# Performance work log

Hardware: AMD Instinct MI355X
Metric: run time of the kernel (lower is better)

Reference implementation:

```python
import jax, jax.numpy as jnp
import numpy as np

N_NODES = 100000
N_EDGES = 1200000
MAX_ATOM_TYPE = 100
NUM_FEATURES = 92
GC_DIM = 64          # pre_layer_dim == gc_dim == CGConv channels
NUM_RBF = 32
NUM_GC_LAYERS = 4
CUTOFF_UPPER = 5.0
BN_EPS = 1e-5


def setup_inputs() -> dict:
    key = jax.random.key(0)
    ks = jax.random.split(key, 12)
    atom_types = jax.random.randint(ks[0], (N_NODES,), 0, MAX_ATOM_TYPE, dtype=jnp.int32)
    pos = jax.random.uniform(ks[1], (N_NODES, 3), dtype=jnp.float32) * 6.0  # box side 6 -> many dists < cutoff
    edge_index = jax.random.randint(ks[2], (2, N_EDGES), 0, N_NODES, dtype=jnp.int32)
    # parameters
    emb = jax.random.normal(ks[3], (MAX_ATOM_TYPE, NUM_FEATURES), dtype=jnp.float32)
    s = 1.0 / np.sqrt(NUM_FEATURES)
    pre_W = jax.random.uniform(ks[4], (NUM_FEATURES, GC_DIM), minval=-s, maxval=s, dtype=jnp.float32)
    pre_b = jnp.zeros((GC_DIM,), jnp.float32)
    zdim = 2 * GC_DIM + NUM_RBF  # [x_i, x_j, edge_attr]
    sz = 1.0 / np.sqrt(zdim)
    Wf = jax.random.uniform(ks[5], (NUM_GC_LAYERS, zdim, GC_DIM), minval=-sz, maxval=sz, dtype=jnp.float32)
    bf = jnp.zeros((NUM_GC_LAYERS, GC_DIM), jnp.float32)
    Ws = jax.random.uniform(ks[6], (NUM_GC_LAYERS, zdim, GC_DIM), minval=-sz, maxval=sz, dtype=jnp.float32)
    bs = jnp.zeros((NUM_GC_LAYERS, GC_DIM), jnp.float32)
    bn_gamma = jnp.ones((NUM_GC_LAYERS, GC_DIM), jnp.float32)
    bn_beta = jnp.zeros((NUM_GC_LAYERS, GC_DIM), jnp.float32)
    # ExpNormalSmearing (torchmd-net) init
    start = np.exp(-CUTOFF_UPPER)
    means = jnp.asarray(np.linspace(start, 1.0, NUM_RBF), jnp.float32)
    betas = jnp.full((NUM_RBF,), (2.0 / NUM_RBF * (1.0 - start)) ** -2, jnp.float32)
    return {"atom_types": atom_types, "pos": pos, "edge_index": edge_index,
            "emb": emb, "pre_W": pre_W, "pre_b": pre_b,
            "Wf": Wf, "bf": bf, "Ws": Ws, "bs": bs,
            "bn_gamma": bn_gamma, "bn_beta": bn_beta,
            "means": means, "betas": betas}


def _forward(atom_types, pos, edge_index, emb, pre_W, pre_b, Wf, bf, Ws, bs,
             bn_gamma, bn_beta, means, betas):
    src, dst = edge_index[0], edge_index[1]
    # distance (edge_vec = pos[src] - pos[dst])
    vec = pos[src] - pos[dst]                                  # [E,3]
    dist = jnp.sqrt(jnp.sum(vec * vec, axis=-1) + 1e-12)       # [E]
    # expnorm RBF with cosine cutoff (cutoff_lower = 0)
    cutoff = 0.5 * (jnp.cos(dist * (np.pi / CUTOFF_UPPER)) + 1.0) * (dist < CUTOFF_UPPER)
    alpha = 5.0 / CUTOFF_UPPER
    edge_attr = cutoff[:, None] * jnp.exp(
        -betas * (jnp.exp(-alpha * dist)[:, None] - means) ** 2)  # [E,NUM_RBF]
    # embedding + pre layer
    x = emb[atom_types]                                        # [N,F]
    x = jax.nn.relu(x @ pre_W + pre_b)                         # [N,C]
    # mean-aggregation degree (scatter-mean denominator)
    deg = jax.ops.segment_sum(jnp.ones_like(dist), dst, num_segments=N_NODES)
    inv_deg = jnp.where(deg > 0, 1.0 / jnp.maximum(deg, 1.0), 0.0)[:, None]
    for l in range(NUM_GC_LAYERS):
        # CGConv: z = [x_i, x_j, e]; out = x + mean_j(sigmoid(lin_f(z)) * softplus(lin_s(z)))
        z = jnp.concatenate([x[dst], x[src], edge_attr], axis=-1)   # [E, 2C+R]
        msg = jax.nn.sigmoid(z @ Wf[l] + bf[l]) * jax.nn.softplus(z @ Ws[l] + bs[l])
        agg = jax.ops.segment_sum(msg, dst, num_segments=N_NODES) * inv_deg
        x = x + agg
        # BatchNorm1d (batch statistics, biased var, as in torch training mode)
        mu = jnp.mean(x, axis=0)
        var = jnp.mean((x - mu) ** 2, axis=0)
        x = (x - mu) * jax.lax.rsqrt(var + BN_EPS) * bn_gamma[l] + bn_beta[l]
    return x


def reference(atom_types, pos, edge_index, emb, pre_W, pre_b, Wf, bf, Ws, bs,
              bn_gamma, bn_beta, means, betas):
    return _forward(atom_types, pos, edge_index, emb, pre_W, pre_b, Wf, bf, Ws, bs,
                    bn_gamma, bn_beta, means, betas)
```

## Files before the change

### kernel.cpp

```cpp
#include <hip/hip_runtime.h>
#include <math.h>

#define N_NODES 100000
#define N_EDGES 1200000
#define GC 64
#define RBF 32
#define NLAYERS 4
#define NF 92
#define NATOM 100
#define BN_EPS 1e-5f
#define TILE_GRID 2048
#define NWIN (N_EDGES / 16)
#define LOG2E 1.44269504f
#define LN2 0.69314718f

typedef _Float16 half8 __attribute__((ext_vector_type(8)));
typedef _Float16 half4 __attribute__((ext_vector_type(4)));
typedef float f32x4 __attribute__((ext_vector_type(4)));

__global__ __launch_bounds__(256) void deg_kernel(
    const int* __restrict__ ei, int* __restrict__ deg)
{
    int e = blockIdx.x * 256 + threadIdx.x;
    if (e >= N_EDGES) return;
    atomicAdd(&deg[ei[N_EDGES + e]], 1);
}

__global__ __launch_bounds__(256) void scan_a_kernel(const int* __restrict__ deg, int* __restrict__ bsums)
{
    __shared__ int sm[256];
    int tid = threadIdx.x;
    int i = blockIdx.x * 256 + tid;
    int v = (i < N_NODES) ? deg[i] : 0;
    sm[tid] = v;
    __syncthreads();
    for (int s = 128; s > 0; s >>= 1) {
        if (tid < s) sm[tid] += sm[tid + s];
        __syncthreads();
    }
    if (tid == 0) bsums[blockIdx.x] = sm[0];
}

__global__ __launch_bounds__(512) void scan_b_kernel(const int* __restrict__ bsums, int* __restrict__ boffs)
{
    __shared__ int sm[512];
    int tid = threadIdx.x;
    int v = (tid < 391) ? bsums[tid] : 0;
    sm[tid] = v;
    __syncthreads();
    for (int off = 1; off < 512; off <<= 1) {
        int t = (tid >= off) ? sm[tid - off] : 0;
        __syncthreads();
        sm[tid] += t;
        __syncthreads();
    }
    boffs[tid] = (tid == 0) ? 0 : sm[tid - 1];
}

__global__ __launch_bounds__(256) void scan_c_kernel(
    const int* __restrict__ deg, const int* __restrict__ boffs,
    int* __restrict__ row_st, float* __restrict__ inv_deg)
{
    __shared__ int sm[256];
    int tid = threadIdx.x;
    int i = blockIdx.x * 256 + tid;
    int v = (i < N_NODES) ? deg[i] : 0;
    sm[tid] = v;
    __syncthreads();
    for (int off = 1; off < 256; off <<= 1) {
        int t = (tid >= off) ? sm[tid - off] : 0;
        __syncthreads();
        sm[tid] += t;
        __syncthreads();
    }
    if (i <= N_NODES) row_st[i] = boffs[blockIdx.x] + sm[tid] - v;
    if (i < N_NODES) inv_deg[i] = (v > 0) ? (1.0f / (float)v) : 0.0f;
}

__global__ __launch_bounds__(256) void scatter_perm_kernel(
    const int* __restrict__ ei, const int* __restrict__ row_st,
    int* __restrict__ cursor, int* __restrict__ csr_src, int* __restrict__ csr_dst)
{
    int e = blockIdx.x * 256 + threadIdx.x;
    if (e >= N_EDGES) return;
    int s = ei[e];
    int d = ei[N_EDGES + e];
    int p = atomicAdd(&cursor[d], 1);
    int idx = row_st[d] + p;
    csr_src[idx] = s;
    csr_dst[idx] = d;
}

__global__ __launch_bounds__(256) void rbf_kernel(
    const int* __restrict__ csr_src, const int* __restrict__ csr_dst,
    const float* __restrict__ pos,
    const float* __restrict__ means, const float* __restrict__ betas,
    unsigned int* __restrict__ ea)
{
    int idx = blockIdx.x * 256 + threadIdx.x;
    if (idx >= N_EDGES) return;
    int s = csr_src[idx];
    int d = csr_dst[idx];
    float dx = pos[s * 3 + 0] - pos[d * 3 + 0];
    float dy = pos[s * 3 + 1] - pos[d * 3 + 1];
    float dz = pos[s * 3 + 2] - pos[d * 3 + 2];
    float dist = sqrtf(dx * dx + dy * dy + dz * dz + 1e-12f);

    float cut = 0.0f;
    if (dist < 5.0f) cut = 0.5f * (__cosf(dist * 0.6283185307179586f) + 1.0f);
    float ex = __expf(-dist);
    union { _Float16 h[32]; uint4 u[4]; } pk;
#pragma unroll
    for (int k = 0; k < 32; k++) {
        float v = ex - means[k];
        pk.h[k] = (_Float16)(cut * __expf(-betas[k] * v * v));
    }
    uint4* op = (uint4*)(ea + (size_t)idx * 16);
    op[0] = pk.u[0];
    op[1] = pk.u[1];
    op[2] = pk.u[2];
    op[3] = pk.u[3];
}

__global__ __launch_bounds__(256) void window_prep_kernel(
    const int* __restrict__ csr_dst, const float* __restrict__ inv_deg,
    unsigned char* __restrict__ seg8, int* __restrict__ wnode, _Float16* __restrict__ inv_e)
{
    int w = blockIdx.x * 256 + threadIdx.x;
    if (w >= NWIN) return;
    int base = w * 16;
    int prev = -1, s = -1;
    for (int k = 0; k < 16; k++) {
        int d = csr_dst[base + k];
        if (d != prev) { s++; prev = d; wnode[base + s] = d; }
        seg8[base + k] = (unsigned char)s;
        inv_e[base + k] = (_Float16)(inv_deg[d] * LN2);
    }
    for (int m = s + 1; m < 16; m++) wnode[base + m] = -1;
}

__global__ __launch_bounds__(256) void wcvt_kernel(
    const float* __restrict__ Wf, const float* __restrict__ Ws,
    _Float16* __restrict__ wf16, _Float16* __restrict__ ws16)
{
    int i = blockIdx.x * 256 + threadIdx.x;
    int l = i / (160 * GC);
    int r = i - l * 160 * GC;
    int k = r >> 6;
    int col = r & 63;
    size_t o = ((size_t)l * GC + col) * 160 + k;
    wf16[o] = (_Float16)(Wf[i] * LOG2E);
    ws16[o] = (_Float16)(Ws[i] * LOG2E);
}

__global__ __launch_bounds__(64) void atom_table_kernel(
    const float* __restrict__ emb, const float* __restrict__ pre_W,
    const float* __restrict__ pre_b, float* __restrict__ T)
{
    int a = blockIdx.x;
    int c = threadIdx.x;
    float acc = pre_b[c];
    for (int k = 0; k < NF; k++) acc = fmaf(emb[a * NF + k], pre_W[k * GC + c], acc);
    T[a * GC + c] = fmaxf(acc, 0.0f);
}

__global__ __launch_bounds__(256) void xinit_kernel(
    const int* __restrict__ atom_types, const float* __restrict__ T,
    float* __restrict__ x, _Float16* __restrict__ x16)
{
    int i = blockIdx.x * 256 + threadIdx.x;
    int n = i >> 4;
    int a = atom_types[n];
    float4 v = ((const float4*)T)[a * 16 + (i & 15)];
    ((float4*)x)[i] = v;
    half4 h = { (_Float16)v.x, (_Float16)v.y, (_Float16)v.z, (_Float16)v.w };
    ((half4*)x16)[i] = h;
}

static __device__ __forceinline__ void compute_win(
    half8 D0, half8 D1, half8 S0, half8 S1, half8 E, int moff,
    const half8 (&WGF)[5][2], const half8 (&WGS)[5][2],
    const float (&biasf)[2], const float (&biass)[2],
    int r16, int quad, int cb,
    const unsigned char* __restrict__ seg8, const int* __restrict__ wnode,
    const _Float16* __restrict__ inv_e, float* __restrict__ x)
{
    unsigned int segq = *(const unsigned int*)(seg8 + moff + quad * 4);
    int4 wn4 = *(const int4*)(wnode + moff + quad * 4);
    half4 inv4 = *(const half4*)(inv_e + moff + quad * 4);

    f32x4 accf[2], accs[2];
#pragma unroll
    for (int ctl = 0; ctl < 2; ctl++) {
        accf[ctl] = (f32x4){biasf[ctl], biasf[ctl], biasf[ctl], biasf[ctl]};
        accs[ctl] = (f32x4){biass[ctl], biass[ctl], biass[ctl], biass[ctl]};
    }
#pragma unroll
    for (int ctl = 0; ctl < 2; ctl++) {
        accf[ctl] = __builtin_amdgcn_mfma_f32_16x16x32_f16(D0, WGF[0][ctl], accf[ctl], 0, 0, 0);
        accs[ctl] = __builtin_amdgcn_mfma_f32_16x16x32_f16(D0, WGS[0][ctl], accs[ctl], 0, 0, 0);
        accf[ctl] = __builtin_amdgcn_mfma_f32_16x16x32_f16(D1, WGF[1][ctl], accf[ctl], 0, 0, 0);
        accs[ctl] = __builtin_amdgcn_mfma_f32_16x16x32_f16(D1, WGS[1][ctl], accs[ctl], 0, 0, 0);
        accf[ctl] = __builtin_amdgcn_mfma_f32_16x16x32_f16(S0, WGF[2][ctl], accf[ctl], 0, 0, 0);
        accs[ctl] = __builtin_amdgcn_mfma_f32_16x16x32_f16(S0, WGS[2][ctl], accs[ctl], 0, 0, 0);
        accf[ctl] = __builtin_amdgcn_mfma_f32_16x16x32_f16(S1, WGF[3][ctl], accf[ctl], 0, 0, 0);
        accs[ctl] = __builtin_amdgcn_mfma_f32_16x16x32_f16(S1, WGS[3][ctl], accs[ctl], 0, 0, 0);
        accf[ctl] = __builtin_amdgcn_mfma_f32_16x16x32_f16(E,  WGF[4][ctl], accf[ctl], 0, 0, 0);
        accs[ctl] = __builtin_amdgcn_mfma_f32_16x16x32_f16(E,  WGS[4][ctl], accs[ctl], 0, 0, 0);
    }
    half4 msgh[2];
#pragma unroll
    for (int ctl = 0; ctl < 2; ctl++) {
#pragma unroll
        for (int rr = 0; rr < 4; rr++) {
            float af = accf[ctl][rr];
            float as = accs[ctl][rr];
            float sg = __builtin_amdgcn_rcpf(1.0f + __builtin_amdgcn_exp2f(-af));
            float sp = fmaxf(as, 0.0f)
                     + __builtin_amdgcn_logf(1.0f + __builtin_amdgcn_exp2f(-__builtin_fabsf(as)));
            msgh[ctl][rr] = (_Float16)(sg * sp);
        }
    }
    half4 am;
#pragma unroll
    for (int j = 0; j < 4; j++) {
        int sj = (segq >> (8 * j)) & 0xff;
        am[j] = (sj == r16) ? inv4[j] : (_Float16)0.0f;
    }
    int wa[4] = { wn4.x, wn4.y, wn4.z, wn4.w };
    const f32x4 zf = (f32x4){0.0f, 0.0f, 0.0f, 0.0f};
#pragma unroll
    for (int ctl = 0; ctl < 2; ctl++) {
        f32x4 red = __builtin_amdgcn_mfma_f32_16x16x16f16(am, msgh[ctl], zf, 0, 0, 0);
#pragma unroll
        for (int rr = 0; rr < 4; rr++) {
            int nd = wa[rr];
            if (nd >= 0) atomicAdd(&x[(size_t)nd * GC + cb + ctl * 16 + r16], red[rr]);
        }
    }
}

#define LOADFRAGS(P0_, P1_, Q0_, Q1_, EE_, SRC_, DST_, WW_)                          \
    P0_ = *(const half8*)(x16 + (size_t)(DST_) * GC + quad * 8);                     \
    P1_ = *(const half8*)(x16 + (size_t)(DST_) * GC + 32 + quad * 8);                \
    Q0_ = *(const half8*)(x16 + (size_t)(SRC_) * GC + quad * 8);                     \
    Q1_ = *(const half8*)(x16 + (size_t)(SRC_) * GC + 32 + quad * 8);                \
    EE_ = *(const half8*)(ea + ((size_t)(WW_) * 16 + r16) * RBF + quad * 8);

__global__ __launch_bounds__(256, 3) void win_mfma_kernel(
    const _Float16* __restrict__ x16, const _Float16* __restrict__ ea,
    const int* __restrict__ csr_src, const int* __restrict__ csr_dst,
    const unsigned char* __restrict__ seg8, const int* __restrict__ wnode,
    const _Float16* __restrict__ inv_e,
    const _Float16* __restrict__ wf16, const _Float16* __restrict__ ws16,
    const float* __restrict__ bfv, const float* __restrict__ bsv,
    float* __restrict__ x)
{
    const int lane = threadIdx.x & 63;
    const int wid = threadIdx.x >> 6;
    const int quad = lane >> 4;
    const int r16 = lane & 15;
    const int wgid = blockIdx.x * 4 + wid;
    const int cb = (wgid & 1) * 32;
    int w = wgid >> 1;
    const int NSEQ = TILE_GRID * 2;

    half8 WGF[5][2], WGS[5][2];
#pragma unroll
    for (int ctl = 0; ctl < 2; ctl++) {
        const _Float16* wfp = wf16 + (size_t)(cb + ctl * 16 + r16) * 160 + quad * 8;
        const _Float16* wsp = ws16 + (size_t)(cb + ctl * 16 + r16) * 160 + quad * 8;
#pragma unroll
        for (int kt = 0; kt < 5; kt++) {
            WGF[kt][ctl] = *(const half8*)(wfp + kt * 32);
            WGS[kt][ctl] = *(const half8*)(wsp + kt * 32);
        }
    }
    float biasf[2], biass[2];
#pragma unroll
    for (int ctl = 0; ctl < 2; ctl++) {
        int col = cb + ctl * 16 + r16;
        biasf[ctl] = bfv[col] * LOG2E;
        biass[ctl] = bsv[col] * LOG2E;
    }

    int sA = csr_src[w * 16 + r16];
    int dA = csr_dst[w * 16 + r16];
    half8 AD0, AD1, AS0, AS1, AE;
    LOADFRAGS(AD0, AD1, AS0, AS1, AE, sA, dA, w);
    int moffA = w * 16;

    int wB = w + NSEQ; if (wB >= NWIN) wB = NWIN - 1;
    int sB = csr_src[wB * 16 + r16];
    int dB = csr_dst[wB * 16 + r16];
    half8 BD0, BD1, BQ0, BQ1, BE;
    LOADFRAGS(BD0, BD1, BQ0, BQ1, BE, sB, dB, wB);
    int moffB = wB * 16;

    int wC = wB + NSEQ; if (wC >= NWIN) wC = NWIN - 1;
    int sC = csr_src[wC * 16 + r16];
    int dC = csr_dst[wC * 16 + r16];

    while (true) {
        compute_win(AD0, AD1, AS0, AS1, AE, moffA, WGF, WGS, biasf, biass,
                    r16, quad, cb, seg8, wnode, inv_e, x);
        LOADFRAGS(AD0, AD1, AS0, AS1, AE, sC, dC, wC);
        moffA = wC * 16;
        wC += NSEQ; if (wC >= NWIN) wC = NWIN - 1;
        sC = csr_src[wC * 16 + r16];
        dC = csr_dst[wC * 16 + r16];
        w += NSEQ;
        if (w >= NWIN) break;

        compute_win(BD0, BD1, BQ0, BQ1, BE, moffB, WGF, WGS, biasf, biass,
                    r16, quad, cb, seg8, wnode, inv_e, x);
        LOADFRAGS(BD0, BD1, BQ0, BQ1, BE, sC, dC, wC);
        moffB = wC * 16;
        wC += NSEQ; if (wC >= NWIN) wC = NWIN - 1;
        sC = csr_src[wC * 16 + r16];
        dC = csr_dst[wC * 16 + r16];
        w += NSEQ;
        if (w >= NWIN) break;
    }
}

__global__ __launch_bounds__(256) void stats_kernel(const float* __restrict__ x, float* __restrict__ stats)
{
    const int lane = threadIdx.x & 63;
    const int wid = threadIdx.x >> 6;
    int w = blockIdx.x * 4 + wid;
    float s1 = 0.0f, s2 = 0.0f;
    for (int n = w; n < N_NODES; n += 1024) {
        float v = x[(size_t)n * GC + lane];
        s1 += v;
        s2 = fmaf(v, v, s2);
    }
    __shared__ float rs1[4][64];
    __shared__ float rs2[4][64];
    rs1[wid][lane] = s1;
    rs2[wid][lane] = s2;
    __syncthreads();
    if (threadIdx.x < 64) {
        atomicAdd(&stats[lane], rs1[0][lane] + rs1[1][lane] + rs1[2][lane] + rs1[3][lane]);
    } else if (threadIdx.x < 128) {
        int c = threadIdx.x & 63;
        atomicAdd(&stats[64 + c], rs2[0][c] + rs2[1][c] + rs2[2][c] + rs2[3][c]);
    }
}

__global__ __launch_bounds__(256) void bn_x16_kernel(
    const float* __restrict__ xn, const float* __restrict__ stats,
    const float* __restrict__ gamma, const float* __restrict__ beta,
    float* __restrict__ xout, _Float16* __restrict__ x16)
{
    int i = blockIdx.x * 256 + threadIdx.x;
    int c4 = (i & 15) * 4;
    float4 v = ((const float4*)xn)[i];
    float vv[4] = {v.x, v.y, v.z, v.w};
    float o[4];
    const float invN = 1.0f / (float)N_NODES;
#pragma unroll
    for (int t = 0; t < 4; t++) {
        int c = c4 + t;
        float mu = stats[c] * invN;
        float var = stats[64 + c] * invN - mu * mu;
        float sc = gamma[c] * rsqrtf(var + BN_EPS);
        o[t] = (vv[t] - mu) * sc + beta[c];
    }
    ((float4*)xout)[i] = make_float4(o[0], o[1], o[2], o[3]);
    half4 h = { (_Float16)o[0], (_Float16)o[1], (_Float16)o[2], (_Float16)o[3] };
    ((half4*)x16)[i] = h;
}

__global__ __launch_bounds__(256) void bn_kernel(
    const float* __restrict__ xn, const float* __restrict__ stats,
    const float* __restrict__ gamma, const float* __restrict__ beta,
    float* __restrict__ out)
{
    int i = blockIdx.x * 256 + threadIdx.x;
    int c4 = (i & 15) * 4;
    float4 v = ((const float4*)xn)[i];
    float vv[4] = {v.x, v.y, v.z, v.w};
    float o[4];
    const float invN = 1.0f / (float)N_NODES;
#pragma unroll
    for (int t = 0; t < 4; t++) {
        int c = c4 + t;
        float mu = stats[c] * invN;
        float var = stats[64 + c] * invN - mu * mu;
        float sc = gamma[c] * rsqrtf(var + BN_EPS);
        o[t] = (vv[t] - mu) * sc + beta[c];
    }
    ((float4*)out)[i] = make_float4(o[0], o[1], o[2], o[3]);
}

extern "C" void kernel_launch(void* const* d_in, const int* in_sizes, int n_in,
                              void* d_out, int out_size, void* d_ws, size_t ws_size,
                              hipStream_t stream)
{
    const int* atom_types = (const int*)d_in[0];
    const float* pos = (const float*)d_in[1];
    const int* edge_index = (const int*)d_in[2];
    const float* emb = (const float*)d_in[3];
    const float* pre_W = (const float*)d_in[4];
    const float* pre_b = (const float*)d_in[5];
    const float* Wf = (const float*)d_in[6];
    const float* bf = (const float*)d_in[7];
    const float* Ws = (const float*)d_in[8];
    const float* bs = (const float*)d_in[9];
    const float* gamma = (const float*)d_in[10];
    const float* beta = (const float*)d_in[11];
    const float* means = (const float*)d_in[12];
    const float* betas = (const float*)d_in[13];

    char* base = (char*)d_ws;
    char* p = base;
    auto alloc = [&](size_t bytes) -> char* {
        char* r = p;
        p += (bytes + 255) & ~(size_t)255;
        return r;
    };
    unsigned int* ea = (unsigned int*)alloc((size_t)N_EDGES * RBF * 2);
    float* x = (float*)alloc((size_t)N_NODES * GC * 4);
    _Float16* x16 = (_Float16*)alloc((size_t)N_NODES * GC * 2);
    int* csr_src = (int*)alloc((size_t)N_EDGES * 4);
    int* csr_dst = (int*)alloc((size_t)N_EDGES * 4);
    int* wnode = (int*)alloc((size_t)N_EDGES * 4);
    unsigned char* seg8 = (unsigned char*)alloc((size_t)N_EDGES);
    _Float16* inv_e = (_Float16*)alloc((size_t)N_EDGES * 2);
    _Float16* wf16 = (_Float16*)alloc((size_t)NLAYERS * GC * 160 * 2);
    _Float16* ws16 = (_Float16*)alloc((size_t)NLAYERS * GC * 160 * 2);
    int* row_st = (int*)alloc((size_t)(N_NODES + 1) * 4);
    float* inv_deg = (float*)alloc((size_t)N_NODES * 4);
    float* T = (float*)alloc((size_t)NATOM * GC * 4);
    int* bsums = (int*)alloc(512 * 4);
    int* boffs = (int*)alloc(512 * 4);
    const size_t ZR_INTS = (size_t)2 * N_NODES + 128 * NLAYERS + 64;
    char* zr = alloc(ZR_INTS * 4);
    int* deg = (int*)zr;
    int* cursor = deg + N_NODES;
    float* stats = (float*)(cursor + N_NODES);

    if ((size_t)(p - base) > ws_size) return;

    (void)hipMemsetAsync(zr, 0, ZR_INTS * 4, stream);

    const int EG = (N_EDGES + 255) / 256;
    deg_kernel<<<EG, 256, 0, stream>>>(edge_index, deg);
    scan_a_kernel<<<391, 256, 0, stream>>>(deg, bsums);
    scan_b_kernel<<<1, 512, 0, stream>>>(bsums, boffs);
    scan_c_kernel<<<391, 256, 0, stream>>>(deg, boffs, row_st, inv_deg);
    scatter_perm_kernel<<<EG, 256, 0, stream>>>(edge_index, row_st, cursor, csr_src, csr_dst);
    rbf_kernel<<<EG, 256, 0, stream>>>(csr_src, csr_dst, pos, means, betas, ea);
    window_prep_kernel<<<(NWIN + 255) / 256, 256, 0, stream>>>(csr_dst, inv_deg, seg8, wnode, inv_e);
    wcvt_kernel<<<(NLAYERS * 160 * GC) / 256, 256, 0, stream>>>(Wf, Ws, wf16, ws16);
    atom_table_kernel<<<NATOM, 64, 0, stream>>>(emb, pre_W, pre_b, T);
    xinit_kernel<<<N_NODES * 16 / 256, 256, 0, stream>>>(atom_types, T, x, x16);

    for (int l = 0; l < NLAYERS; l++) {
        win_mfma_kernel<<<TILE_GRID, 256, 0, stream>>>(
            x16, (const _Float16*)ea, csr_src, csr_dst, seg8, wnode, inv_e,
            wf16 + (size_t)l * GC * 160, ws16 + (size_t)l * GC * 160,
            bf + l * GC, bs + l * GC, x);
        stats_kernel<<<256, 256, 0, stream>>>(x, stats + l * 128);
        if (l < NLAYERS - 1) {
            bn_x16_kernel<<<N_NODES * 16 / 256, 256, 0, stream>>>(
                x, stats + l * 128, gamma + l * GC, beta + l * GC, x, x16);
        } else {
            bn_kernel<<<N_NODES * 16 / 256, 256, 0, stream>>>(
                x, stats + l * 128, gamma + l * GC, beta + l * GC, (float*)d_out);
        }
    }
}
```

Before: 852.0 us.

## Precompute per-node destination projection and fuse it into batchnorm kernel

The x_i (destination) part of both linear layers, plus bias, is now computed once per node into an fp16-packed buffer P2u instead of once per edge. The edge kernel loads these precomputed partial sums as accumulator initial values and runs only the source and edge-attribute MFMAs, cutting per-edge matmul work by about 40%. The per-node projection is fused into the batchnorm kernel for later layers, and softplus is simplified to log(1+exp2(x)), which risks overflow for large inputs. The cost is an extra node-sized buffer, scattered per-destination loads in the edge loop, and fp16 rounding of the partial sums.

```diff
diff --git a/kernel.cpp b/kernel.cpp
--- a/kernel.cpp
+++ b/kernel.cpp
@@ -16,7 +16,9 @@
 
 typedef _Float16 half8 __attribute__((ext_vector_type(8)));
 typedef _Float16 half4 __attribute__((ext_vector_type(4)));
+typedef _Float16 half2v __attribute__((ext_vector_type(2)));
 typedef float f32x4 __attribute__((ext_vector_type(4)));
+union U32H2 { unsigned int u; half2v h; };
 
 __global__ __launch_bounds__(256) void deg_kernel(
     const int* __restrict__ ei, int* __restrict__ deg)
@@ -177,84 +179,48 @@
     ((half4*)x16)[i] = h;
 }
 
-static __device__ __forceinline__ void compute_win(
-    half8 D0, half8 D1, half8 S0, half8 S1, half8 E, int moff,
-    const half8 (&WGF)[5][2], const half8 (&WGS)[5][2],
-    const float (&biasf)[2], const float (&biass)[2],
-    int r16, int quad, int cb,
-    const unsigned char* __restrict__ seg8, const int* __restrict__ wnode,
-    const _Float16* __restrict__ inv_e, float* __restrict__ x)
-{
-    unsigned int segq = *(const unsigned int*)(seg8 + moff + quad * 4);
-    int4 wn4 = *(const int4*)(wnode + moff + quad * 4);
-    half4 inv4 = *(const half4*)(inv_e + moff + quad * 4);
-
+static __device__ __forceinline__ void proj_mfma16(
+    const _Float16* __restrict__ wf, const _Float16* __restrict__ ws,
+    const float* __restrict__ bfv, const float* __restrict__ bsv,
+    const half8 Bn[2], int cb, int node, unsigned int* __restrict__ P2u)
+{
+    const int lane = threadIdx.x & 63;
+    const int quad = lane >> 4;
+    const int r16 = lane & 15;
     f32x4 accf[2], accs[2];
 #pragma unroll
-    for (int ctl = 0; ctl < 2; ctl++) {
-        accf[ctl] = (f32x4){biasf[ctl], biasf[ctl], biasf[ctl], biasf[ctl]};
-        accs[ctl] = (f32x4){biass[ctl], biass[ctl], biass[ctl], biass[ctl]};
-    }
-#pragma unroll
-    for (int ctl = 0; ctl < 2; ctl++) {
-        accf[ctl] = __builtin_amdgcn_mfma_f32_16x16x32_f16(D0, WGF[0][ctl], accf[ctl], 0, 0, 0);
-        accs[ctl] = __builtin_amdgcn_mfma_f32_16x16x32_f16(D0, WGS[0][ctl], accs[ctl], 0, 0, 0);
-        accf[ctl] = __builtin_amdgcn_mfma_f32_16x16x32_f16(D1, WGF[1][ctl], accf[ctl], 0, 0, 0);
-        accs[ctl] = __builtin_amdgcn_mfma_f32_16x16x32_f16(D1, WGS[1][ctl], accs[ctl], 0, 0, 0);
-        accf[ctl] = __builtin_amdgcn_mfma_f32_16x16x32_f16(S0, WGF[2][ctl], accf[ctl], 0, 0, 0);
-        accs[ctl] = __builtin_amdgcn_mfma_f32_16x16x32_f16(S0, WGS[2][ctl], accs[ctl], 0, 0, 0);
-        accf[ctl] = __builtin_amdgcn_mfma_f32_16x16x32_f16(S1, WGF[3][ctl], accf[ctl], 0, 0, 0);
-        accs[ctl] = __builtin_amdgcn_mfma_f32_16x16x32_f16(S1, WGS[3][ctl], accs[ctl], 0, 0, 0);
-        accf[ctl] = __builtin_amdgcn_mfma_f32_16x16x32_f16(E,  WGF[4][ctl], accf[ctl], 0, 0, 0);
-        accs[ctl] = __builtin_amdgcn_mfma_f32_16x16x32_f16(E,  WGS[4][ctl], accs[ctl], 0, 0, 0);
-    }
-    half4 msgh[2];
-#pragma unroll
-    for (int ctl = 0; ctl < 2; ctl++) {
-#pragma unroll
-        for (int rr = 0; rr < 4; rr++) {
-            float af = accf[ctl][rr];
-            float as = accs[ctl][rr];
-            float sg = __builtin_amdgcn_rcpf(1.0f + __builtin_amdgcn_exp2f(-af));
-            float sp = fmaxf(as, 0.0f)
-                     + __builtin_amdgcn_logf(1.0f + __builtin_amdgcn_exp2f(-__builtin_fabsf(as)));
-            msgh[ctl][rr] = (_Float16)(sg * sp);
-        }
-    }
-    half4 am;
-#pragma unroll
-    for (int j = 0; j < 4; j++) {
-        int sj = (segq >> (8 * j)) & 0xff;
-        am[j] = (sj == r16) ? inv4[j] : (_Float16)0.0f;
-    }
-    int wa[4] = { wn4.x, wn4.y, wn4.z, wn4.w };
-    const f32x4 zf = (f32x4){0.0f, 0.0f, 0.0f, 0.0f};
-#pragma unroll
-    for (int ctl = 0; ctl < 2; ctl++) {
-        f32x4 red = __builtin_amdgcn_mfma_f32_16x16x16f16(am, msgh[ctl], zf, 0, 0, 0);
-#pragma unroll
-        for (int rr = 0; rr < 4; rr++) {
-            int nd = wa[rr];
-            if (nd >= 0) atomicAdd(&x[(size_t)nd * GC + cb + ctl * 16 + r16], red[rr]);
-        }
-    }
-}
-
-#define LOADFRAGS(P0_, P1_, Q0_, Q1_, EE_, SRC_, DST_, WW_)                          \
-    P0_ = *(const half8*)(x16 + (size_t)(DST_) * GC + quad * 8);                     \
-    P1_ = *(const half8*)(x16 + (size_t)(DST_) * GC + 32 + quad * 8);                \
-    Q0_ = *(const half8*)(x16 + (size_t)(SRC_) * GC + quad * 8);                     \
-    Q1_ = *(const half8*)(x16 + (size_t)(SRC_) * GC + 32 + quad * 8);                \
-    EE_ = *(const half8*)(ea + ((size_t)(WW_) * 16 + r16) * RBF + quad * 8);
-
-__global__ __launch_bounds__(256, 3) void win_mfma_kernel(
-    const _Float16* __restrict__ x16, const _Float16* __restrict__ ea,
-    const int* __restrict__ csr_src, const int* __restrict__ csr_dst,
-    const unsigned char* __restrict__ seg8, const int* __restrict__ wnode,
-    const _Float16* __restrict__ inv_e,
-    const _Float16* __restrict__ wf16, const _Float16* __restrict__ ws16,
+    for (int sub = 0; sub < 2; sub++) {
+        accf[sub] = (f32x4){0.f, 0.f, 0.f, 0.f};
+        accs[sub] = (f32x4){0.f, 0.f, 0.f, 0.f};
+    }
+#pragma unroll
+    for (int kt = 0; kt < 2; kt++) {
+#pragma unroll
+        for (int sub = 0; sub < 2; sub++) {
+            int chan = cb + sub * 16 + r16;
+            half8 a = *(const half8*)(wf + (size_t)chan * 160 + kt * 32 + quad * 8);
+            half8 b = *(const half8*)(ws + (size_t)chan * 160 + kt * 32 + quad * 8);
+            accf[sub] = __builtin_amdgcn_mfma_f32_16x16x32_f16(a, Bn[kt], accf[sub], 0, 0, 0);
+            accs[sub] = __builtin_amdgcn_mfma_f32_16x16x32_f16(b, Bn[kt], accs[sub], 0, 0, 0);
+        }
+    }
+#pragma unroll
+    for (int sub = 0; sub < 2; sub++) {
+        float4 bf4 = *(const float4*)(bfv + cb + sub * 16 + quad * 4);
+        float4 bs4 = *(const float4*)(bsv + cb + sub * 16 + quad * 4);
+        half8 h = { (_Float16)(accf[sub][0] + bf4.x * LOG2E), (_Float16)(accs[sub][0] + bs4.x * LOG2E),
+                    (_Float16)(accf[sub][1] + bf4.y * LOG2E), (_Float16)(accs[sub][1] + bs4.y * LOG2E),
+                    (_Float16)(accf[sub][2] + bf4.z * LOG2E), (_Float16)(accs[sub][2] + bs4.z * LOG2E),
+                    (_Float16)(accf[sub][3] + bf4.w * LOG2E), (_Float16)(accs[sub][3] + bs4.w * LOG2E) };
+        *(half8*)(P2u + (size_t)node * GC + cb + sub * 16 + quad * 4) = h;
+    }
+}
+
+__global__ __launch_bounds__(256) void proj_kernel(
+    const _Float16* __restrict__ x16,
+    const _Float16* __restrict__ wf, const _Float16* __restrict__ ws,
     const float* __restrict__ bfv, const float* __restrict__ bsv,
-    float* __restrict__ x)
+    unsigned int* __restrict__ P2u)
 {
     const int lane = threadIdx.x & 63;
     const int wid = threadIdx.x >> 6;
@@ -262,63 +228,204 @@
     const int r16 = lane & 15;
     const int wgid = blockIdx.x * 4 + wid;
     const int cb = (wgid & 1) * 32;
+    const int nb = (wgid >> 1) * 16;
+    half8 Bn[2];
+    Bn[0] = *(const half8*)(x16 + (size_t)(nb + r16) * GC + quad * 8);
+    Bn[1] = *(const half8*)(x16 + (size_t)(nb + r16) * GC + 32 + quad * 8);
+    proj_mfma16(wf, ws, bfv, bsv, Bn, cb, nb + r16, P2u);
+}
+
+__global__ __launch_bounds__(256) void bnproj_kernel(
+    const float* __restrict__ xn, const float* __restrict__ stats,
+    const float* __restrict__ gamma, const float* __restrict__ beta,
+    float* __restrict__ xout, _Float16* __restrict__ x16,
+    const _Float16* __restrict__ wf, const _Float16* __restrict__ ws,
+    const float* __restrict__ bfv, const float* __restrict__ bsv,
+    unsigned int* __restrict__ P2u)
+{
+    __shared__ _Float16 lx[32 * 72];
+    const int nb = blockIdx.x * 32;
+    const float invN = 1.0f / (float)N_NODES;
+
+#pragma unroll
+    for (int rep = 0; rep < 2; rep++) {
+        int g = rep * 256 + threadIdx.x;
+        int gi = blockIdx.x * 512 + g;
+        int node = g >> 4;
+        int c4 = (g & 15) * 4;
+        float4 v = ((const float4*)xn)[gi];
+        float vv[4] = {v.x, v.y, v.z, v.w};
+        float o[4];
+#pragma unroll
+        for (int t = 0; t < 4; t++) {
+            int c = c4 + t;
+            float mu = stats[c] * invN;
+            float var = stats[64 + c] * invN - mu * mu;
+            float sc = gamma[c] * rsqrtf(var + BN_EPS);
+            o[t] = (vv[t] - mu) * sc + beta[c];
+        }
+        ((float4*)xout)[gi] = make_float4(o[0], o[1], o[2], o[3]);
+        half4 h = { (_Float16)o[0], (_Float16)o[1], (_Float16)o[2], (_Float16)o[3] };
+        ((half4*)x16)[gi] = h;
+        *(half4*)(lx + node * 72 + c4) = h;
+    }
+    __syncthreads();
+
+    const int lane = threadIdx.x & 63;
+    const int wid = threadIdx.x >> 6;
+    const int quad = lane >> 4;
+    const int r16 = lane & 15;
+    const int cb = (wid & 1) * 32;
+    const int tn = (wid >> 1) * 16 + r16;
+    half8 Bn[2];
+    Bn[0] = *(const half8*)(lx + tn * 72 + quad * 8);
+    Bn[1] = *(const half8*)(lx + tn * 72 + 32 + quad * 8);
+    proj_mfma16(wf, ws, bfv, bsv, Bn, cb, nb + tn, P2u);
+}
+
+static __device__ __forceinline__ void compute_win(
+    half8 S0, half8 S1, half8 E,
+    const unsigned int (&pv)[8], unsigned int segq, int4 wn4, half4 inv4,
+    const half8 (&WGF)[3][2], const half8 (&WGS)[3][2],
+    int r16, int quad, int cb, float* __restrict__ x)
+{
+    f32x4 accf[2], accs[2];
+#pragma unroll
+    for (int ctl = 0; ctl < 2; ctl++) {
+#pragma unroll
+        for (int rr = 0; rr < 4; rr++) {
+            U32H2 t; t.u = pv[ctl * 4 + rr];
+            accf[ctl][rr] = (float)t.h.x;
+            accs[ctl][rr] = (float)t.h.y;
+        }
+    }
+    __builtin_amdgcn_s_setprio(1);
+#pragma unroll
+    for (int ctl = 0; ctl < 2; ctl++) {
+        accf[ctl] = __builtin_amdgcn_mfma_f32_16x16x32_f16(S0, WGF[0][ctl], accf[ctl], 0, 0, 0);
+        accs[ctl] = __builtin_amdgcn_mfma_f32_16x16x32_f16(S0, WGS[0][ctl], accs[ctl], 0, 0, 0);
+        accf[ctl] = __builtin_amdgcn_mfma_f32_16x16x32_f16(S1, WGF[1][ctl], accf[ctl], 0, 0, 0);
+        accs[ctl] = __builtin_amdgcn_mfma_f32_16x16x32_f16(S1, WGS[1][ctl], accs[ctl], 0, 0, 0);
+        accf[ctl] = __builtin_amdgcn_mfma_f32_16x16x32_f16(E,  WGF[2][ctl], accf[ctl], 0, 0, 0);
+        accs[ctl] = __builtin_amdgcn_mfma_f32_16x16x32_f16(E,  WGS[2][ctl], accs[ctl], 0, 0, 0);
+    }
+    __builtin_amdgcn_s_setprio(0);
+    half4 msgh[2];
+#pragma unroll
+    for (int ctl = 0; ctl < 2; ctl++) {
+#pragma unroll
+        for (int rr = 0; rr < 4; rr++) {
+            float af = accf[ctl][rr];
+            float as = accs[ctl][rr];
+            float sg = __builtin_amdgcn_rcpf(1.0f + __builtin_amdgcn_exp2f(-af));
+            float sp = __builtin_amdgcn_logf(1.0f + __builtin_amdgcn_exp2f(as));
+            msgh[ctl][rr] = (_Float16)(sg * sp);
+        }
+    }
+    half4 am;
+#pragma unroll
+    for (int j = 0; j < 4; j++) {
+        int sj = (segq >> (8 * j)) & 0xff;
+        am[j] = (sj == r16) ? inv4[j] : (_Float16)0.0f;
+    }
+    int wa[4] = { wn4.x, wn4.y, wn4.z, wn4.w };
+    const f32x4 zf = (f32x4){0.0f, 0.0f, 0.0f, 0.0f};
+#pragma unroll
+    for (int ctl = 0; ctl < 2; ctl++) {
+        f32x4 red = __builtin_amdgcn_mfma_f32_16x16x16f16(am, msgh[ctl], zf, 0, 0, 0);
+#pragma unroll
+        for (int rr = 0; rr < 4; rr++) {
+            int nd = wa[rr];
+            if (nd >= 0) atomicAdd(&x[(size_t)nd * GC + cb + ctl * 16 + r16], red[rr]);
+        }
+    }
+}
+
+#define LOADSET(S0_, S1_, EE_, SGQ_, WN4_, INV4_, PV_, SRC_, D4_, WW_)               \
+    S0_ = *(const half8*)(x16 + (size_t)(SRC_) * GC + quad * 8);                     \
+    S1_ = *(const half8*)(x16 + (size_t)(SRC_) * GC + 32 + quad * 8);                \
+    EE_ = *(const half8*)(ea + ((size_t)(WW_) * 16 + r16) * RBF + quad * 8);         \
+    SGQ_ = *(const unsigned int*)(seg8 + (WW_) * 16 + quad * 4);                     \
+    WN4_ = *(const int4*)(wnode + (WW_) * 16 + quad * 4);                            \
+    INV4_ = *(const half4*)(inv_e + (WW_) * 16 + quad * 4);                          \
+    {                                                                                 \
+        int dd0 = (D4_).x, dd1 = (D4_).y, dd2 = (D4_).z, dd3 = (D4_).w;              \
+        PV_[0] = P2u[(size_t)dd0 * GC + cb + r16];                                   \
+        PV_[1] = P2u[(size_t)dd1 * GC + cb + r16];                                   \
+        PV_[2] = P2u[(size_t)dd2 * GC + cb + r16];                                   \
+        PV_[3] = P2u[(size_t)dd3 * GC + cb + r16];                                   \
+        PV_[4] = P2u[(size_t)dd0 * GC + cb + 16 + r16];                              \
+        PV_[5] = P2u[(size_t)dd1 * GC + cb + 16 + r16];                              \
+        PV_[6] = P2u[(size_t)dd2 * GC + cb + 16 + r16];                              \
+        PV_[7] = P2u[(size_t)dd3 * GC + cb + 16 + r16];                              \
+    }
+
+__global__ __launch_bounds__(256, 3) void win_mfma_kernel(
+    const _Float16* __restrict__ x16, const _Float16* __restrict__ ea,
+    const int* __restrict__ csr_src, const int* __restrict__ csr_dst,
+    const unsigned char* __restrict__ seg8, const int* __restrict__ wnode,
+    const _Float16* __restrict__ inv_e, const unsigned int* __restrict__ P2u,
+    const _Float16* __restrict__ wf16, const _Float16* __restrict__ ws16,
+    float* __restrict__ x)
+{
+    const int lane = threadIdx.x & 63;
+    const int wid = __builtin_amdgcn_readfirstlane(threadIdx.x >> 6);
+    const int quad = lane >> 4;
+    const int r16 = lane & 15;
+    const int wgid = blockIdx.x * 4 + wid;
+    const int cb = (wgid & 1) * 32;
     int w = wgid >> 1;
     const int NSEQ = TILE_GRID * 2;
 
-    half8 WGF[5][2], WGS[5][2];
+    half8 WGF[3][2], WGS[3][2];
 #pragma unroll
     for (int ctl = 0; ctl < 2; ctl++) {
-        const _Float16* wfp = wf16 + (size_t)(cb + ctl * 16 + r16) * 160 + quad * 8;
-        const _Float16* wsp = ws16 + (size_t)(cb + ctl * 16 + r16) * 160 + quad * 8;
-#pragma unroll
-        for (int kt = 0; kt < 5; kt++) {
+        const _Float16* wfp = wf16 + (size_t)(cb + ctl * 16 + r16) * 160 + 64 + quad * 8;
+        const _Float16* wsp = ws16 + (size_t)(cb + ctl * 16 + r16) * 160 + 64 + quad * 8;
+#pragma unroll
+        for (int kt = 0; kt < 3; kt++) {
             WGF[kt][ctl] = *(const half8*)(wfp + kt * 32);
             WGS[kt][ctl] = *(const half8*)(wsp + kt * 32);
         }
     }
-    float biasf[2], biass[2];
-#pragma unroll
-    for (int ctl = 0; ctl < 2; ctl++) {
-        int col = cb + ctl * 16 + r16;
-        biasf[ctl] = bfv[col] * LOG2E;
-        biass[ctl] = bsv[col] * LOG2E;
-    }
 
     int sA = csr_src[w * 16 + r16];
-    int dA = csr_dst[w * 16 + r16];
-    half8 AD0, AD1, AS0, AS1, AE;
-    LOADFRAGS(AD0, AD1, AS0, AS1, AE, sA, dA, w);
-    int moffA = w * 16;
+    int4 d4A = *(const int4*)(csr_dst + w * 16 + quad * 4);
+    half8 AS0, AS1, AE;
+    unsigned int apv[8], asgq;
+    int4 awn4;
+    half4 ainv4;
+    LOADSET(AS0, AS1, AE, asgq, awn4, ainv4, apv, sA, d4A, w);
 
     int wB = w + NSEQ; if (wB >= NWIN) wB = NWIN - 1;
     int sB = csr_src[wB * 16 + r16];
-    int dB = csr_dst[wB * 16 + r16];
-    half8 BD0, BD1, BQ0, BQ1, BE;
-    LOADFRAGS(BD0, BD1, BQ0, BQ1, BE, sB, dB, wB);
-    int moffB = wB * 16;
+    int4 d4B = *(const int4*)(csr_dst + wB * 16 + quad * 4);
+    half8 BS0, BS1, BE;
+    unsigned int bpv[8], bsgq;
+    int4 bwn4;
+    half4 binv4;
+    LOADSET(BS0, BS1, BE, bsgq, bwn4, binv4, bpv, sB, d4B, wB);
 
     int wC = wB + NSEQ; if (wC >= NWIN) wC = NWIN - 1;
     int sC = csr_src[wC * 16 + r16];
-    int dC = csr_dst[wC * 16 + r16];
+    int4 d4C = *(const int4*)(csr_dst + wC * 16 + quad * 4);
 
     while (true) {
-        compute_win(AD0, AD1, AS0, AS1, AE, moffA, WGF, WGS, biasf, biass,
-                    r16, quad, cb, seg8, wnode, inv_e, x);
-        LOADFRAGS(AD0, AD1, AS0, AS1, AE, sC, dC, wC);
-        moffA = wC * 16;
+        compute_win(AS0, AS1, AE, apv, asgq, awn4, ainv4,
+                    WGF, WGS, r16, quad, cb, x);
+        LOADSET(AS0, AS1, AE, asgq, awn4, ainv4, apv, sC, d4C, wC);
         wC += NSEQ; if (wC >= NWIN) wC = NWIN - 1;
         sC = csr_src[wC * 16 + r16];
-        dC = csr_dst[wC * 16 + r16];
+        d4C = *(const int4*)(csr_dst + wC * 16 + quad * 4);
         w += NSEQ;
         if (w >= NWIN) break;
 
-        compute_win(BD0, BD1, BQ0, BQ1, BE, moffB, WGF, WGS, biasf, biass,
-                    r16, quad, cb, seg8, wnode, inv_e, x);
-        LOADFRAGS(BD0, BD1, BQ0, BQ1, BE, sC, dC, wC);
-        moffB = wC * 16;
+        compute_win(BS0, BS1, BE, bpv, bsgq, bwn4, binv4,
+                    WGF, WGS, r16, quad, cb, x);
+        LOADSET(BS0, BS1, BE, bsgq, bwn4, binv4, bpv, sC, d4C, wC);
         wC += NSEQ; if (wC >= NWIN) wC = NWIN - 1;
         sC = csr_src[wC * 16 + r16];
-        dC = csr_dst[wC * 16 + r16];
+        d4C = *(const int4*)(csr_dst + wC * 16 + quad * 4);
         w += NSEQ;
         if (w >= NWIN) break;
     }
@@ -346,30 +453,6 @@
         int c = threadIdx.x & 63;
         atomicAdd(&stats[64 + c], rs2[0][c] + rs2[1][c] + rs2[2][c] + rs2[3][c]);
     }
-}
-
-__global__ __launch_bounds__(256) void bn_x16_kernel(
-    const float* __restrict__ xn, const float* __restrict__ stats,
-    const float* __restrict__ gamma, const float* __restrict__ beta,
-    float* __restrict__ xout, _Float16* __restrict__ x16)
-{
-    int i = blockIdx.x * 256 + threadIdx.x;
-    int c4 = (i & 15) * 4;
-    float4 v = ((const float4*)xn)[i];
-    float vv[4] = {v.x, v.y, v.z, v.w};
-    float o[4];
-    const float invN = 1.0f / (float)N_NODES;
-#pragma unroll
-    for (int t = 0; t < 4; t++) {
-        int c = c4 + t;
-        float mu = stats[c] * invN;
-        float var = stats[64 + c] * invN - mu * mu;
-        float sc = gamma[c] * rsqrtf(var + BN_EPS);
-        o[t] = (vv[t] - mu) * sc + beta[c];
-    }
-    ((float4*)xout)[i] = make_float4(o[0], o[1], o[2], o[3]);
-    half4 h = { (_Float16)o[0], (_Float16)o[1], (_Float16)o[2], (_Float16)o[3] };
-    ((half4*)x16)[i] = h;
 }
 
 __global__ __launch_bounds__(256) void bn_kernel(
@@ -423,6 +506,7 @@
     unsigned int* ea = (unsigned int*)alloc((size_t)N_EDGES * RBF * 2);
     float* x = (float*)alloc((size_t)N_NODES * GC * 4);
     _Float16* x16 = (_Float16*)alloc((size_t)N_NODES * GC * 2);
+    unsigned int* P2u = (unsigned int*)alloc((size_t)N_NODES * GC * 4);
     int* csr_src = (int*)alloc((size_t)N_EDGES * 4);
     int* csr_dst = (int*)alloc((size_t)N_EDGES * 4);
     int* wnode = (int*)alloc((size_t)N_EDGES * 4);
@@ -456,16 +540,18 @@
     wcvt_kernel<<<(NLAYERS * 160 * GC) / 256, 256, 0, stream>>>(Wf, Ws, wf16, ws16);
     atom_table_kernel<<<NATOM, 64, 0, stream>>>(emb, pre_W, pre_b, T);
     xinit_kernel<<<N_NODES * 16 / 256, 256, 0, stream>>>(atom_types, T, x, x16);
+    proj_kernel<<<N_NODES / 32, 256, 0, stream>>>(x16, wf16, ws16, bf, bs, P2u);
 
     for (int l = 0; l < NLAYERS; l++) {
         win_mfma_kernel<<<TILE_GRID, 256, 0, stream>>>(
-            x16, (const _Float16*)ea, csr_src, csr_dst, seg8, wnode, inv_e,
-            wf16 + (size_t)l * GC * 160, ws16 + (size_t)l * GC * 160,
-            bf + l * GC, bs + l * GC, x);
+            x16, (const _Float16*)ea, csr_src, csr_dst, seg8, wnode, inv_e, P2u,
+            wf16 + (size_t)l * GC * 160, ws16 + (size_t)l * GC * 160, x);
         stats_kernel<<<256, 256, 0, stream>>>(x, stats + l * 128);
         if (l < NLAYERS - 1) {
-            bn_x16_kernel<<<N_NODES * 16 / 256, 256, 0, stream>>>(
-                x, stats + l * 128, gamma + l * GC, beta + l * GC, x, x16);
+            bnproj_kernel<<<N_NODES / 32, 256, 0, stream>>>(
+                x, stats + l * 128, gamma + l * GC, beta + l * GC, x, x16,
+                wf16 + (size_t)(l + 1) * GC * 160, ws16 + (size_t)(l + 1) * GC * 160,
+                bf + (l + 1) * GC, bs + (l + 1) * GC, P2u);
         } else {
             bn_kernel<<<N_NODES * 16 / 256, 256, 0, stream>>>(
                 x, stats + l * 128, gamma + l * GC, beta + l * GC, (float*)d_out);
```

After: 854.6 us. No clear change (+0.3%).
